# Optimization experiments

Measured on AMD Instinct MI355X. Metric: run time of the kernel, lower is better.

Reference implementation:

```python
import jax, jax.numpy as jnp
import numpy as np

D_MODEL = 1024
NUM_HEADS = 16
D_IN = 1024

def setup_inputs() -> dict:
    key = jax.random.key(0)
    ks = jax.random.split(key, 5)
    scale = 1.0 / np.sqrt(D_IN)
    return {
        "in_features": jax.random.normal(ks[0], (4, 2048, D_IN), dtype=jnp.float32),
        "q_weight": jax.random.normal(ks[1], (D_MODEL, D_IN), dtype=jnp.float32) * scale,
        "k_weight": jax.random.normal(ks[2], (D_MODEL, D_IN), dtype=jnp.float32) * scale,
        "v_weight": jax.random.normal(ks[3], (D_MODEL, D_IN), dtype=jnp.float32) * scale,
        "o_weight": jax.random.normal(ks[4], (D_MODEL, D_MODEL), dtype=jnp.float32) * scale,
    }

def reference(in_features, q_weight, k_weight, v_weight, o_weight):
    batch, seq_len, _ = in_features.shape
    d_head = D_MODEL // NUM_HEADS
    # QKV projections (Linear with no bias: x @ W^T)
    q = jnp.einsum('bsi,di->bsd', in_features, q_weight)
    k = jnp.einsum('bsi,di->bsd', in_features, k_weight)
    v = jnp.einsum('bsi,di->bsd', in_features, v_weight)
    # split heads -> [b, h, s, d_head]
    q = q.reshape(batch, seq_len, NUM_HEADS, d_head).transpose(0, 2, 1, 3)
    k = k.reshape(batch, seq_len, NUM_HEADS, d_head).transpose(0, 2, 1, 3)
    v = v.reshape(batch, seq_len, NUM_HEADS, d_head).transpose(0, 2, 1, 3)
    # scaled dot-product attention (scale by per-head dim, as in SelfAttention)
    scores = jnp.einsum('bhqd,bhkd->bhqk', q, k) / jnp.sqrt(jnp.float32(d_head))
    probs = jax.nn.softmax(scores, axis=-1)
    ctx = jnp.einsum('bhqk,bhkd->bhqd', probs, v)
    # merge heads -> [b, s, d_model]
    ctx = ctx.transpose(0, 2, 1, 3).reshape(batch, seq_len, D_MODEL)
    # output projection
    return jnp.einsum('bsd,md->bsm', ctx, o_weight)
```

## Files before the change

### kernel.cpp

```cpp
#include <hip/hip_runtime.h>

typedef _Float16 half8 __attribute__((ext_vector_type(8)));
typedef _Float16 half4v __attribute__((ext_vector_type(4)));
typedef __fp16 fp16x2 __attribute__((ext_vector_type(2)));
typedef float f32x4 __attribute__((ext_vector_type(4)));
typedef float f32x16 __attribute__((ext_vector_type(16)));

__device__ __forceinline__ void gload_lds16(const _Float16* g, _Float16* l) {
    __builtin_amdgcn_global_load_lds(
        (const __attribute__((address_space(1))) void*)g,
        (__attribute__((address_space(3))) void*)l,
        16, 0, 0);
}

__global__ void cvt_f32_f16(const float* __restrict__ src, _Float16* __restrict__ dst, int n4) {
    int i = blockIdx.x * blockDim.x + threadIdx.x;
    if (i >= n4) return;
    f32x4 v = ((const f32x4*)src)[i];
    half4v h;
    h[0] = (_Float16)v[0]; h[1] = (_Float16)v[1];
    h[2] = (_Float16)v[2]; h[3] = (_Float16)v[3];
    ((half4v*)dst)[i] = h;
}

__global__ void cvt4_f32_f16(const float* __restrict__ s0, const float* __restrict__ s1,
                             const float* __restrict__ s2, const float* __restrict__ s3,
                             _Float16* __restrict__ dst) {
    int i = blockIdx.x * blockDim.x + threadIdx.x;
    int wsel = blockIdx.y;
    const float* src = (wsel == 0) ? s0 : (wsel == 1) ? s1 : (wsel == 2) ? s2 : s3;
    f32x4 v = ((const f32x4*)src)[i];
    half4v h;
    h[0] = (_Float16)v[0]; h[1] = (_Float16)v[1];
    h[2] = (_Float16)v[2]; h[3] = (_Float16)v[3];
    ((half4v*)(dst + (size_t)wsel * 1048576))[i] = h;
}

template<int MODE>
__global__ __launch_bounds__(256, 2)
void gemm_nt(const _Float16* __restrict__ A,
             const _Float16* __restrict__ Wbase,
             void* __restrict__ outbase)
{
    __shared__ _Float16 lds[32768];
    _Float16* Asb = lds;
    _Float16* Bsb = lds + 16384;

    const int tid  = threadIdx.x;
    const int lane = tid & 63;
    const int w    = tid >> 6;
    const int wr   = w >> 1, wc = w & 1;
    const int lr   = lane & 15, lg = lane >> 4;
    const int brow = blockIdx.x * 128;
    const int bcol = blockIdx.y * 128;
    const int mat  = (MODE == 0) ? blockIdx.z : 0;

    const _Float16* Ap = A + (size_t)brow * 1024;
    const _Float16* Bp = Wbase + (size_t)mat * (1024u * 1024u) + (size_t)bcol * 1024;

    const int srw  = tid >> 2;
    const int sch  = tid & 3;
    const int soff = ((sch ^ (srw & 3)) << 3);

    auto stage = [&](int buf, int kt) {
#pragma unroll
        for (int i = 0; i < 2; ++i) {
            const int ra = i * 64 + srw;
            gload_lds16(Ap + (size_t)ra * 1024 + kt * 32 + soff,
                        Asb + buf * 4096 + i * 2048 + w * 512);
            gload_lds16(Bp + (size_t)ra * 1024 + kt * 32 + soff,
                        Bsb + buf * 4096 + i * 2048 + w * 512);
        }
    };

    f32x4 acc[4][4] = {};
    const int swz = ((lg ^ (lr & 3)) << 3);

    stage(0, 0);
    stage(1, 1);
    asm volatile("s_waitcnt vmcnt(4)" ::: "memory");
    __builtin_amdgcn_s_barrier();
    __builtin_amdgcn_sched_barrier(0);

    for (int t = 0; t < 32; ++t) {
        if (t < 30) stage((t + 2) & 3, t + 2);
        const _Float16* Ab = Asb + (t & 3) * 4096;
        const _Float16* Bb = Bsb + (t & 3) * 4096;
        half8 af[4], bf[4];
#pragma unroll
        for (int mi = 0; mi < 4; ++mi)
            af[mi] = *(const half8*)&Ab[(wr * 64 + mi * 16 + lr) * 32 + swz];
#pragma unroll
        for (int ni = 0; ni < 4; ++ni)
            bf[ni] = *(const half8*)&Bb[(wc * 64 + ni * 16 + lr) * 32 + swz];
        __builtin_amdgcn_s_setprio(1);
#pragma unroll
        for (int mi = 0; mi < 4; ++mi)
#pragma unroll
            for (int ni = 0; ni < 4; ++ni)
                acc[mi][ni] = __builtin_amdgcn_mfma_f32_16x16x32_f16(af[mi], bf[ni], acc[mi][ni], 0, 0, 0);
        __builtin_amdgcn_s_setprio(0);
        if (t < 30)       { asm volatile("s_waitcnt vmcnt(4)" ::: "memory"); }
        else if (t == 30) { asm volatile("s_waitcnt vmcnt(0)" ::: "memory"); }
        if (t < 31) {
            __builtin_amdgcn_s_barrier();
            __builtin_amdgcn_sched_barrier(0);
        }
    }

    if (MODE == 0) {
        _Float16* outp = (_Float16*)outbase + (size_t)mat * (8192u * 1024u);
        if (mat == 2) {
            _Float16* Ts = lds;
#pragma unroll
            for (int p = 0; p < 2; ++p) {
                __syncthreads();
                if (wc == p) {
#pragma unroll
                    for (int mi = 0; mi < 4; ++mi)
#pragma unroll
                        for (int ni = 0; ni < 4; ++ni) {
                            int drow = ni * 16 + lr;
                            int s0   = wr * 64 + mi * 16 + lg * 4;
                            half4v o;
#pragma unroll
                            for (int r = 0; r < 4; ++r) o[r] = (_Float16)acc[mi][ni][r];
                            int byteoff = drow * 256 + s0 * 2;
                            byteoff ^= (drow & 7) << 4;
                            *(half4v*)((char*)Ts + byteoff) = o;
                        }
                }
                __syncthreads();
                {
                    int row   = tid >> 2;
                    int cbase = (tid & 3) * 4;
                    int gd = bcol + p * 64 + row;
                    int h = gd >> 6, dd = gd & 63;
                    int b = brow >> 11, sseq = brow & 2047;
                    _Float16* gout = outp + (((size_t)b * 16 + h) * 64 + dd) * 2048 + sseq;
#pragma unroll
                    for (int j = 0; j < 4; ++j) {
                        int c  = cbase + j;
                        int lc = c ^ (row & 7);
                        half8 v = *(const half8*)&Ts[row * 128 + lc * 8];
                        *(half8*)&gout[c * 8] = v;
                    }
                }
            }
        } else {
            const float scale = (mat == 0) ? 0.18033688f : 1.0f;
#pragma unroll
            for (int mi = 0; mi < 4; ++mi)
#pragma unroll
                for (int ni = 0; ni < 4; ++ni)
#pragma unroll
                    for (int r = 0; r < 4; ++r) {
                        int row = brow + wr * 64 + mi * 16 + lg * 4 + r;
                        int col = bcol + wc * 64 + ni * 16 + lr;
                        int b = row >> 11, s = row & 2047;
                        int h = col >> 6,  d = col & 63;
                        outp[(((size_t)b * 16 + h) * 2048 + s) * 64 + d] =
                            (_Float16)(acc[mi][ni][r] * scale);
                    }
        }
    } else {
        float* outp = (float*)outbase;
#pragma unroll
        for (int mi = 0; mi < 4; ++mi)
#pragma unroll
            for (int ni = 0; ni < 4; ++ni)
#pragma unroll
                for (int r = 0; r < 4; ++r) {
                    int row = brow + wr * 64 + mi * 16 + lg * 4 + r;
                    int col = bcol + wc * 64 + ni * 16 + lr;
                    outp[(size_t)row * 1024 + col] = acc[mi][ni][r];
                }
    }
}

#define M_FIX 10.0f
__global__ __launch_bounds__(256, 4)
void attn_kernel(const _Float16* __restrict__ Q,
                 const _Float16* __restrict__ Kx,
                 const _Float16* __restrict__ Vt,
                 _Float16* __restrict__ Ctx)
{
    __shared__ _Float16 Ks[2][64 * 72];
    __shared__ _Float16 Vs[2][64 * 72];

    const int tid = threadIdx.x, lane = tid & 63, w = tid >> 6;
    const int l31 = lane & 31, hi = lane >> 5;

    const int wg = blockIdx.x;
    const int j = ((wg & 7) << 7) + (wg >> 3);
    const int bh = j >> 4, qblk = j & 15;

    const _Float16* Qp  = Q  + ((size_t)bh * 2048 + qblk * 128) * 64;
    const _Float16* Kp  = Kx + (size_t)bh * 2048 * 64;
    const _Float16* Vtp = Vt + (size_t)bh * 64 * 2048;

    half8 qf[4];
#pragma unroll
    for (int ks = 0; ks < 4; ++ks)
        qf[ks] = *(const half8*)(Qp + (size_t)(w * 32 + l31) * 64 + ks * 16 + hi * 8);

    const int srow = tid >> 3;
    const int scol = (tid & 7) * 8;
    const _Float16* Kg0 = Kp  + (size_t)srow * 64   + scol;
    const _Float16* Vg0 = Vtp + (size_t)srow * 2048 + scol;
    const int ldso = srow * 72 + scol;

    const fp16x2 ones2 = {(__fp16)1.0f, (__fp16)1.0f};

    f32x16 cacc[2] = {};
    float l0 = 0.f, l1 = 0.f;

    half8 kr0, kr1, vr0, vr1;
    kr0 = *(const half8*)(Kg0);
    kr1 = *(const half8*)(Kg0 + 2048);
    vr0 = *(const half8*)(Vg0);
    vr1 = *(const half8*)(Vg0 + 32 * 2048);
    *(half8*)&Ks[0][ldso]           = kr0;
    *(half8*)&Ks[0][ldso + 32 * 72] = kr1;
    *(half8*)&Vs[0][ldso]           = vr0;
    *(half8*)&Vs[0][ldso + 32 * 72] = vr1;
    __syncthreads();

    for (int t = 0; t < 32; ++t) {
        const int cur = t & 1;
        if (t < 31) {
            kr0 = *(const half8*)(Kg0 + (size_t)(t + 1) * 4096);
            kr1 = *(const half8*)(Kg0 + (size_t)(t + 1) * 4096 + 2048);
        }

        f32x16 sf[2];
        __builtin_amdgcn_s_setprio(1);
#pragma unroll
        for (int kt = 0; kt < 2; ++kt) {
            f32x16 z;
#pragma unroll
            for (int r = 0; r < 16; ++r) z[r] = -M_FIX;
#pragma unroll
            for (int ks = 0; ks < 4; ++ks) {
                half8 kf = *(const half8*)&Ks[cur][(kt * 32 + l31) * 72 + ks * 16 + hi * 8];
                z = __builtin_amdgcn_mfma_f32_32x32x16_f16(kf, qf[ks], z, 0, 0, 0);
            }
            sf[kt] = z;
        }
        __builtin_amdgcn_s_setprio(0);

        if (t < 31) {
            *(half8*)&Ks[cur ^ 1][ldso]           = kr0;
            *(half8*)&Ks[cur ^ 1][ldso + 32 * 72] = kr1;
            vr0 = *(const half8*)(Vg0 + (t + 1) * 64);
            vr1 = *(const half8*)(Vg0 + (t + 1) * 64 + 32 * 2048);
        }

        half8 bf[4];
#pragma unroll
        for (int kt = 0; kt < 2; ++kt) {
#pragma unroll
            for (int r = 0; r < 16; ++r)
                sf[kt][r] = __builtin_amdgcn_exp2f(sf[kt][r]);

            unsigned uq[4][2];
#pragma unroll
            for (int qd = 0; qd < 4; ++qd)
#pragma unroll
                for (int w2 = 0; w2 < 2; ++w2)
                    uq[qd][w2] = __builtin_bit_cast(unsigned,
                        __builtin_amdgcn_cvt_pkrtz(sf[kt][4 * qd + 2 * w2],
                                                   sf[kt][4 * qd + 2 * w2 + 1]));

#pragma unroll
            for (int k1 = 0; k1 < 2; ++k1) {
                union { half8 h; unsigned u[4]; } bu;
#pragma unroll
                for (int w2 = 0; w2 < 2; ++w2) {
                    unsigned a = uq[2 * k1][w2];
                    unsigned b = uq[2 * k1 + 1][w2];
                    asm("v_permlane32_swap_b32 %0, %1" : "+v"(a), "+v"(b));
                    bu.u[w2]     = a;
                    bu.u[2 + w2] = b;
                }
                l0 = __builtin_amdgcn_fdot2(__builtin_bit_cast(fp16x2, bu.u[0]), ones2, l0, false);
                l1 = __builtin_amdgcn_fdot2(__builtin_bit_cast(fp16x2, bu.u[1]), ones2, l1, false);
                l0 = __builtin_amdgcn_fdot2(__builtin_bit_cast(fp16x2, bu.u[2]), ones2, l0, false);
                l1 = __builtin_amdgcn_fdot2(__builtin_bit_cast(fp16x2, bu.u[3]), ones2, l1, false);
                bf[kt * 2 + k1] = bu.h;
            }
        }

        __builtin_amdgcn_s_setprio(1);
#pragma unroll
        for (int dt = 0; dt < 2; ++dt)
#pragma unroll
            for (int ks = 0; ks < 4; ++ks) {
                half8 vf = *(const half8*)&Vs[cur][(dt * 32 + l31) * 72 + ks * 16 + hi * 8];
                cacc[dt] = __builtin_amdgcn_mfma_f32_32x32x16_f16(vf, bf[ks], cacc[dt], 0, 0, 0);
            }
        __builtin_amdgcn_s_setprio(0);

        if (t < 31) {
            *(half8*)&Vs[cur ^ 1][ldso]           = vr0;
            *(half8*)&Vs[cur ^ 1][ldso + 32 * 72] = vr1;
        }
        __syncthreads();
    }

    float l = l0 + l1;
    const float inv = 1.0f / (l + __shfl_xor(l, 32, 64));
    const int s = qblk * 128 + w * 32 + l31;
    _Float16* Cp = Ctx + ((size_t)(bh >> 4) * 2048 + s) * 1024 + (bh & 15) * 64;
#pragma unroll
    for (int dt = 0; dt < 2; ++dt)
#pragma unroll
        for (int qd = 0; qd < 4; ++qd) {
            half4v o;
#pragma unroll
            for (int j2 = 0; j2 < 4; ++j2) o[j2] = (_Float16)(cacc[dt][4 * qd + j2] * inv);
            *(half4v*)&Cp[dt * 32 + qd * 8 + hi * 4] = o;
        }
}

extern "C" void kernel_launch(void* const* d_in, const int* in_sizes, int n_in,
                              void* d_out, int out_size, void* d_ws, size_t ws_size,
                              hipStream_t stream)
{
    const float* X  = (const float*)d_in[0];
    const float* Wq = (const float*)d_in[1];
    const float* Wk = (const float*)d_in[2];
    const float* Wv = (const float*)d_in[3];
    const float* Wo = (const float*)d_in[4];

    if (ws_size < (size_t)(8 + 4 + 24) * 1024 * 1024 * 2) return;
    _Float16* Xh  = (_Float16*)d_ws;
    _Float16* Wh  = Xh + (size_t)8 * 1024 * 1024;
    _Float16* QKV = Wh + (size_t)4 * 1024 * 1024;
    _Float16* Ctx = Xh;

    cvt_f32_f16<<<8192, 256, 0, stream>>>(X, Xh, 2097152);
    cvt4_f32_f16<<<dim3(1024, 4), 256, 0, stream>>>(Wq, Wk, Wv, Wo, Wh);

    gemm_nt<0><<<dim3(64, 8, 3), 256, 0, stream>>>(Xh, Wh, QKV);

    attn_kernel<<<1024, 256, 0, stream>>>(QKV, QKV + 8388608, QKV + 16777216, Ctx);

    gemm_nt<1><<<dim3(64, 8, 1), 256, 0, stream>>>(Ctx, Wh + 3145728, d_out);
}
```

Before: 193.3 us.

## Process two 32-row query groups per wave in attention kernel

Each wave now handles 64 query rows (two groups of 32) instead of 32, so a workgroup covers 256 queries and the grid halves to 512 blocks. Every K/V tile loaded into LDS is reused across twice as many queries, which halves global K/V traffic and the LDS staging and barrier work per query. The cost is higher register pressure (launch bounds lowered from 4 to 2 waves per SIMD) and fewer workgroups to spread across the GPU's compute units.

```diff
diff --git a/kernel.cpp b/kernel.cpp
--- a/kernel.cpp
+++ b/kernel.cpp
@@ -179,7 +179,7 @@
 }
 
 #define M_FIX 10.0f
-__global__ __launch_bounds__(256, 4)
+__global__ __launch_bounds__(256, 2)
 void attn_kernel(const _Float16* __restrict__ Q,
                  const _Float16* __restrict__ Kx,
                  const _Float16* __restrict__ Vt,
@@ -192,17 +192,19 @@
     const int l31 = lane & 31, hi = lane >> 5;
 
     const int wg = blockIdx.x;
-    const int j = ((wg & 7) << 7) + (wg >> 3);
-    const int bh = j >> 4, qblk = j & 15;
-
-    const _Float16* Qp  = Q  + ((size_t)bh * 2048 + qblk * 128) * 64;
+    const int j = ((wg & 7) << 6) + (wg >> 3);
+    const int bh = j >> 3, qblk = j & 7;
+
+    const _Float16* Qp  = Q  + ((size_t)bh * 2048 + qblk * 256) * 64;
     const _Float16* Kp  = Kx + (size_t)bh * 2048 * 64;
     const _Float16* Vtp = Vt + (size_t)bh * 64 * 2048;
 
-    half8 qf[4];
-#pragma unroll
-    for (int ks = 0; ks < 4; ++ks)
-        qf[ks] = *(const half8*)(Qp + (size_t)(w * 32 + l31) * 64 + ks * 16 + hi * 8);
+    half8 qf[2][4];
+#pragma unroll
+    for (int g = 0; g < 2; ++g)
+#pragma unroll
+        for (int ks = 0; ks < 4; ++ks)
+            qf[g][ks] = *(const half8*)(Qp + (size_t)(w * 64 + g * 32 + l31) * 64 + ks * 16 + hi * 8);
 
     const int srow = tid >> 3;
     const int scol = (tid & 7) * 8;
@@ -212,8 +214,8 @@
 
     const fp16x2 ones2 = {(__fp16)1.0f, (__fp16)1.0f};
 
-    f32x16 cacc[2] = {};
-    float l0 = 0.f, l1 = 0.f;
+    f32x16 cacc[2][2] = {};
+    float lp[2][2] = {};
 
     half8 kr0, kr1, vr0, vr1;
     kr0 = *(const half8*)(Kg0);
@@ -233,20 +235,22 @@
             kr1 = *(const half8*)(Kg0 + (size_t)(t + 1) * 4096 + 2048);
         }
 
-        f32x16 sf[2];
+        f32x16 sf[2][2];
         __builtin_amdgcn_s_setprio(1);
 #pragma unroll
-        for (int kt = 0; kt < 2; ++kt) {
-            f32x16 z;
-#pragma unroll
-            for (int r = 0; r < 16; ++r) z[r] = -M_FIX;
-#pragma unroll
-            for (int ks = 0; ks < 4; ++ks) {
-                half8 kf = *(const half8*)&Ks[cur][(kt * 32 + l31) * 72 + ks * 16 + hi * 8];
-                z = __builtin_amdgcn_mfma_f32_32x32x16_f16(kf, qf[ks], z, 0, 0, 0);
+        for (int g = 0; g < 2; ++g)
+#pragma unroll
+            for (int kt = 0; kt < 2; ++kt) {
+                f32x16 z;
+#pragma unroll
+                for (int r = 0; r < 16; ++r) z[r] = -M_FIX;
+#pragma unroll
+                for (int ks = 0; ks < 4; ++ks) {
+                    half8 kf = *(const half8*)&Ks[cur][(kt * 32 + l31) * 72 + ks * 16 + hi * 8];
+                    z = __builtin_amdgcn_mfma_f32_32x32x16_f16(kf, qf[g][ks], z, 0, 0, 0);
+                }
+                sf[g][kt] = z;
             }
-            sf[kt] = z;
-        }
         __builtin_amdgcn_s_setprio(0);
 
         if (t < 31) {
@@ -256,50 +260,53 @@
             vr1 = *(const half8*)(Vg0 + (t + 1) * 64 + 32 * 2048);
         }
 
-        half8 bf[4];
-#pragma unroll
-        for (int kt = 0; kt < 2; ++kt) {
-#pragma unroll
-            for (int r = 0; r < 16; ++r)
-                sf[kt][r] = __builtin_amdgcn_exp2f(sf[kt][r]);
-
-            unsigned uq[4][2];
-#pragma unroll
-            for (int qd = 0; qd < 4; ++qd)
-#pragma unroll
-                for (int w2 = 0; w2 < 2; ++w2)
-                    uq[qd][w2] = __builtin_bit_cast(unsigned,
-                        __builtin_amdgcn_cvt_pkrtz(sf[kt][4 * qd + 2 * w2],
-                                                   sf[kt][4 * qd + 2 * w2 + 1]));
-
-#pragma unroll
-            for (int k1 = 0; k1 < 2; ++k1) {
-                union { half8 h; unsigned u[4]; } bu;
-#pragma unroll
-                for (int w2 = 0; w2 < 2; ++w2) {
-                    unsigned a = uq[2 * k1][w2];
-                    unsigned b = uq[2 * k1 + 1][w2];
-                    asm("v_permlane32_swap_b32 %0, %1" : "+v"(a), "+v"(b));
-                    bu.u[w2]     = a;
-                    bu.u[2 + w2] = b;
-                }
-                l0 = __builtin_amdgcn_fdot2(__builtin_bit_cast(fp16x2, bu.u[0]), ones2, l0, false);
-                l1 = __builtin_amdgcn_fdot2(__builtin_bit_cast(fp16x2, bu.u[1]), ones2, l1, false);
-                l0 = __builtin_amdgcn_fdot2(__builtin_bit_cast(fp16x2, bu.u[2]), ones2, l0, false);
-                l1 = __builtin_amdgcn_fdot2(__builtin_bit_cast(fp16x2, bu.u[3]), ones2, l1, false);
-                bf[kt * 2 + k1] = bu.h;
+#pragma unroll
+        for (int g = 0; g < 2; ++g) {
+            half8 bf[4];
+#pragma unroll
+            for (int kt = 0; kt < 2; ++kt) {
+#pragma unroll
+                for (int r = 0; r < 16; ++r)
+                    sf[g][kt][r] = __builtin_amdgcn_exp2f(sf[g][kt][r]);
+
+                unsigned uq[4][2];
+#pragma unroll
+                for (int qd = 0; qd < 4; ++qd)
+#pragma unroll
+                    for (int w2 = 0; w2 < 2; ++w2)
+                        uq[qd][w2] = __builtin_bit_cast(unsigned,
+                            __builtin_amdgcn_cvt_pkrtz(sf[g][kt][4 * qd + 2 * w2],
+                                                       sf[g][kt][4 * qd + 2 * w2 + 1]));
+
+#pragma unroll
+                for (int k1 = 0; k1 < 2; ++k1) {
+                    union { half8 h; unsigned u[4]; } bu;
+#pragma unroll
+                    for (int w2 = 0; w2 < 2; ++w2) {
+                        unsigned a = uq[2 * k1][w2];
+                        unsigned b = uq[2 * k1 + 1][w2];
+                        asm("v_permlane32_swap_b32 %0, %1" : "+v"(a), "+v"(b));
+                        bu.u[w2]     = a;
+                        bu.u[2 + w2] = b;
+                    }
+                    lp[g][0] = __builtin_amdgcn_fdot2(__builtin_bit_cast(fp16x2, bu.u[0]), ones2, lp[g][0], false);
+                    lp[g][1] = __builtin_amdgcn_fdot2(__builtin_bit_cast(fp16x2, bu.u[1]), ones2, lp[g][1], false);
+                    lp[g][0] = __builtin_amdgcn_fdot2(__builtin_bit_cast(fp16x2, bu.u[2]), ones2, lp[g][0], false);
+                    lp[g][1] = __builtin_amdgcn_fdot2(__builtin_bit_cast(fp16x2, bu.u[3]), ones2, lp[g][1], false);
+                    bf[kt * 2 + k1] = bu.h;
+                }
             }
-        }
-
-        __builtin_amdgcn_s_setprio(1);
-#pragma unroll
-        for (int dt = 0; dt < 2; ++dt)
-#pragma unroll
-            for (int ks = 0; ks < 4; ++ks) {
-                half8 vf = *(const half8*)&Vs[cur][(dt * 32 + l31) * 72 + ks * 16 + hi * 8];
-                cacc[dt] = __builtin_amdgcn_mfma_f32_32x32x16_f16(vf, bf[ks], cacc[dt], 0, 0, 0);
-            }
-        __builtin_amdgcn_s_setprio(0);
+
+            __builtin_amdgcn_s_setprio(1);
+#pragma unroll
+            for (int dt = 0; dt < 2; ++dt)
+#pragma unroll
+                for (int ks = 0; ks < 4; ++ks) {
+                    half8 vf = *(const half8*)&Vs[cur][(dt * 32 + l31) * 72 + ks * 16 + hi * 8];
+                    cacc[g][dt] = __builtin_amdgcn_mfma_f32_32x32x16_f16(vf, bf[ks], cacc[g][dt], 0, 0, 0);
+                }
+            __builtin_amdgcn_s_setprio(0);
+        }
 
         if (t < 31) {
             *(half8*)&Vs[cur ^ 1][ldso]           = vr0;
@@ -308,19 +315,22 @@
         __syncthreads();
     }
 
-    float l = l0 + l1;
-    const float inv = 1.0f / (l + __shfl_xor(l, 32, 64));
-    const int s = qblk * 128 + w * 32 + l31;
-    _Float16* Cp = Ctx + ((size_t)(bh >> 4) * 2048 + s) * 1024 + (bh & 15) * 64;
-#pragma unroll
-    for (int dt = 0; dt < 2; ++dt)
-#pragma unroll
-        for (int qd = 0; qd < 4; ++qd) {
-            half4v o;
-#pragma unroll
-            for (int j2 = 0; j2 < 4; ++j2) o[j2] = (_Float16)(cacc[dt][4 * qd + j2] * inv);
-            *(half4v*)&Cp[dt * 32 + qd * 8 + hi * 4] = o;
-        }
+#pragma unroll
+    for (int g = 0; g < 2; ++g) {
+        float l = lp[g][0] + lp[g][1];
+        const float inv = 1.0f / (l + __shfl_xor(l, 32, 64));
+        const int s = qblk * 256 + w * 64 + g * 32 + l31;
+        _Float16* Cp = Ctx + ((size_t)(bh >> 4) * 2048 + s) * 1024 + (bh & 15) * 64;
+#pragma unroll
+        for (int dt = 0; dt < 2; ++dt)
+#pragma unroll
+            for (int qd = 0; qd < 4; ++qd) {
+                half4v o;
+#pragma unroll
+                for (int j2 = 0; j2 < 4; ++j2) o[j2] = (_Float16)(cacc[g][dt][4 * qd + j2] * inv);
+                *(half4v*)&Cp[dt * 32 + qd * 8 + hi * 4] = o;
+            }
+    }
 }
 
 extern "C" void kernel_launch(void* const* d_in, const int* in_sizes, int n_in,
@@ -344,7 +354,7 @@
 
     gemm_nt<0><<<dim3(64, 8, 3), 256, 0, stream>>>(Xh, Wh, QKV);
 
-    attn_kernel<<<1024, 256, 0, stream>>>(QKV, QKV + 8388608, QKV + 16777216, Ctx);
+    attn_kernel<<<512, 256, 0, stream>>>(QKV, QKV + 8388608, QKV + 16777216, Ctx);
 
     gemm_nt<1><<<dim3(64, 8, 1), 256, 0, stream>>>(Ctx, Wh + 3145728, d_out);
 }
```

After: 188.7 us. 1.02x faster.
